# Optimization experiments

Hardware: AMD Instinct MI355X
Metric: run time of the kernel (lower is better)

The kernel has to match this reference:

```python
import jax, jax.numpy as jnp
import numpy as np

B, T, D, H, L, R, V = 4, 1024, 1024, 16, 12, 32, 50257
HD = D // H
SCALING = 2.0   # lora_alpha(64) / lora_rank(32) at the default 16-bit precision
EPS = 1e-5
KV_QMAX = float(2 ** 8 - 1)  # kv_cache_bits = 8 (middle of [4,8,16])


def _ln(x, g, b):
    m = jnp.mean(x, -1, keepdims=True)
    v = jnp.mean(jnp.square(x - m), -1, keepdims=True)
    return (x - m) * jax.lax.rsqrt(v + EPS) * g + b


def _round_ste(x):
    return x + jax.lax.stop_gradient(jnp.round(x) - x)


def _fake_quant(x, mn, mx):
    # asymmetric learnable fake-quant with straight-through rounding
    scale = (mx - mn) / KV_QMAX
    zp = _round_ste(-mn / scale)
    q = jnp.clip(_round_ste(x / scale) + zp, 0.0, KV_QMAX)
    return (q - zp) * scale


def _sp_linear(x, w, b, la, lb):
    # quantized-base linear (full precision at 16-bit) + LoRA adapter (eval: no dropout)
    return x @ w + b + SCALING * ((x @ la) @ lb)


def setup_inputs() -> dict:
    key = jax.random.key(0)
    ks = iter(jax.random.split(key, 64))
    rn = lambda shape, s=0.02: jax.random.normal(next(ks), shape, jnp.float32) * s
    return {
        "input_ids": jax.random.randint(next(ks), (B, T), 0, V),
        "wte": rn((V, D)), "wpe": rn((T, D)),
        "ln1_g": jnp.ones((L, D)), "ln1_b": jnp.zeros((L, D)),
        "attn_w": rn((L, D, 3 * D)), "attn_b": jnp.zeros((L, 3 * D)),
        "attn_la": rn((L, D, R)), "attn_lb": rn((L, R, 3 * D)),
        "proj_w": rn((L, D, D)), "proj_b": jnp.zeros((L, D)),
        "proj_la": rn((L, D, R)), "proj_lb": rn((L, R, D)),
        "ln2_g": jnp.ones((L, D)), "ln2_b": jnp.zeros((L, D)),
        "fc_w": rn((L, D, 4 * D)), "fc_b": jnp.zeros((L, 4 * D)),
        "fc_la": rn((L, D, R)), "fc_lb": rn((L, R, 4 * D)),
        "mproj_w": rn((L, 4 * D, D)), "mproj_b": jnp.zeros((L, D)),
        "mproj_la": rn((L, 4 * D, R)), "mproj_lb": rn((L, R, D)),
        "kv_min": jnp.full((L,), -4.0), "kv_max": jnp.full((L,), 4.0),
        "lnf_g": jnp.ones((D,)), "lnf_b": jnp.zeros((D,)),
    }


def reference(input_ids, wte, wpe, ln1_g, ln1_b, attn_w, attn_b, attn_la, attn_lb,
              proj_w, proj_b, proj_la, proj_lb, ln2_g, ln2_b, fc_w, fc_b, fc_la,
              fc_lb, mproj_w, mproj_b, mproj_la, mproj_lb, kv_min, kv_max,
              lnf_g, lnf_b):
    mask = jnp.tril(jnp.ones((T, T), bool))
    h = wte[input_ids] + wpe[None, :T]  # [B,T,D] (dropout is identity in eval)

    def block(h, p):
        (g1, b1, aw, ab, ala, alb, pw, pb, pla, plb, g2, b2,
         fw, fb, fla, flb, mw, mb, mla, mlb, mn, mx) = p
        x = _ln(h, g1, b1)
        qkv = _sp_linear(x, aw, ab, ala, alb)  # [B,T,3D]
        q, k, v = jnp.split(qkv, 3, axis=-1)
        heads = lambda t: t.reshape(B, T, H, HD).transpose(0, 2, 1, 3)  # bhtd
        q, k, v = heads(q), heads(k), heads(v)
        # KV-cache fake quantization (default precision flag unset on attn)
        k = _fake_quant(k, mn, mx)
        v = _fake_quant(v, mn, mx)
        att = jnp.einsum('bhqd,bhkd->bhqk', q, k) / np.float32(np.sqrt(HD))
        att = jax.nn.softmax(jnp.where(mask, att, -jnp.inf), axis=-1)
        o = jnp.einsum('bhqk,bhkd->bhqd', att, v).transpose(0, 2, 1, 3).reshape(B, T, D)
        h = h + _sp_linear(o, pw, pb, pla, plb)
        x = _ln(h, g2, b2)
        m = jax.nn.gelu(_sp_linear(x, fw, fb, fla, flb), approximate=False)
        h = h + _sp_linear(m, mw, mb, mla, mlb)
        return h, None

    params = (ln1_g, ln1_b, attn_w, attn_b, attn_la, attn_lb, proj_w, proj_b,
              proj_la, proj_lb, ln2_g, ln2_b, fc_w, fc_b, fc_la, fc_lb,
              mproj_w, mproj_b, mproj_la, mproj_lb, kv_min, kv_max)
    h, _ = jax.lax.scan(block, h, params)
    return _ln(h, lnf_g, lnf_b)
```

## Files before the change

kernel.cpp:

```cpp
#include <hip/hip_runtime.h>
#include <hip/hip_bf16.h>


typedef __bf16 bf16x8 __attribute__((ext_vector_type(8)));
typedef float f32x4 __attribute__((ext_vector_type(4)));

static __device__ __forceinline__ float bf2f(unsigned short u) {
    union { unsigned int i; float f; } c; c.i = ((unsigned int)u) << 16; return c.f;
}
static __device__ __forceinline__ unsigned short f2bf(float f) {
    unsigned int u = __float_as_uint(f);
    u += 0x7fffu + ((u >> 16) & 1u);
    return (unsigned short)(u >> 16);
}

#define GL2LDS(g, l) __builtin_amdgcn_global_load_lds( \
    (const __attribute__((address_space(1))) unsigned int*)(g), \
    (__attribute__((address_space(3))) unsigned int*)(l), 16, 0, 0)

__global__ __launch_bounds__(256) void k_embed(const int* __restrict__ ids,
        const float* __restrict__ wte, const float* __restrict__ wpe,
        float* __restrict__ h) {
    int row = blockIdx.x;
    int t = row & 1023;
    int id = ids[row];
    int d = threadIdx.x * 4;
    float4 a = *(const float4*)(wte + (size_t)id * 1024 + d);
    float4 b = *(const float4*)(wpe + (size_t)t * 1024 + d);
    float4 o = make_float4(a.x + b.x, a.y + b.y, a.z + b.z, a.w + b.w);
    *(float4*)(h + (size_t)row * 1024 + d) = o;
}

template <bool BF16OUT>
__global__ __launch_bounds__(256) void k_ln(const float* __restrict__ h,
        const float* __restrict__ g, const float* __restrict__ be,
        unsigned short* __restrict__ xo, float* __restrict__ fo) {
    int row = blockIdx.x, tid = threadIdx.x;
    float4 v = *(const float4*)(h + (size_t)row * 1024 + tid * 4);
    float s = v.x + v.y + v.z + v.w;
    for (int off = 32; off; off >>= 1) s += __shfl_down(s, off);
    __shared__ float red[8];
    int wid = tid >> 6, lane = tid & 63;
    if (!lane) red[wid] = s;
    __syncthreads();
    float mean = (red[0] + red[1] + red[2] + red[3]) * (1.f / 1024.f);
    float dx = v.x - mean, dy = v.y - mean, dz = v.z - mean, dw = v.w - mean;
    float q = dx * dx + dy * dy + dz * dz + dw * dw;
    for (int off = 32; off; off >>= 1) q += __shfl_down(q, off);
    if (!lane) red[4 + wid] = q;
    __syncthreads();
    float var = (red[4] + red[5] + red[6] + red[7]) * (1.f / 1024.f);
    float inv = 1.0f / sqrtf(var + 1e-5f);
    float4 gv = *(const float4*)(g + tid * 4);
    float4 bv = *(const float4*)(be + tid * 4);
    float y0 = dx * inv * gv.x + bv.x;
    float y1 = dy * inv * gv.y + bv.y;
    float y2 = dz * inv * gv.z + bv.z;
    float y3 = dw * inv * gv.w + bv.w;
    if (BF16OUT) {
        ushort4 o;
        o.x = f2bf(y0); o.y = f2bf(y1); o.z = f2bf(y2); o.w = f2bf(y3);
        *(ushort4*)(xo + (size_t)row * 1024 + tid * 4) = o;
    } else {
        *(float4*)(fo + (size_t)row * 1024 + tid * 4) = make_float4(y0, y1, y2, y3);
    }
}

__global__ __launch_bounds__(256) void k_lora_mfma(const unsigned short* __restrict__ A,
        const unsigned short* __restrict__ laT, unsigned short* __restrict__ tmp, int K) {
    int rowBase = blockIdx.x * 16;
    int tid = threadIdx.x, w = tid >> 6, lane = tid & 63;
    int lrow = lane & 15, lk8 = (lane >> 4) * 8;
    int kq = K >> 2;
    f32x4 acc0 = {0.f, 0.f, 0.f, 0.f}, acc1 = {0.f, 0.f, 0.f, 0.f};
    const unsigned short* arow = A + (size_t)(rowBase + lrow) * K + w * kq + lk8;
    const unsigned short* b0p = laT + (size_t)lrow * K + w * kq + lk8;
    const unsigned short* b1p = laT + (size_t)(16 + lrow) * K + w * kq + lk8;
#pragma unroll 2
    for (int kt = 0; kt < kq; kt += 32) {
        bf16x8 af = *(const bf16x8*)(arow + kt);
        bf16x8 b0 = *(const bf16x8*)(b0p + kt);
        bf16x8 b1 = *(const bf16x8*)(b1p + kt);
        acc0 = __builtin_amdgcn_mfma_f32_16x16x32_bf16(af, b0, acc0, 0, 0, 0);
        acc1 = __builtin_amdgcn_mfma_f32_16x16x32_bf16(af, b1, acc1, 0, 0, 0);
    }
    __shared__ f32x4 red[2][4][64];
    red[0][w][lane] = acc0;
    red[1][w][lane] = acc1;
    __syncthreads();
    if (w == 0) {
        acc0 = red[0][0][lane] + red[0][1][lane] + red[0][2][lane] + red[0][3][lane];
        acc1 = red[1][0][lane] + red[1][1][lane] + red[1][2][lane] + red[1][3][lane];
        int lq = lane >> 4;
#pragma unroll
        for (int rg = 0; rg < 4; ++rg) {
            int row = rowBase + lq * 4 + rg;
            tmp[(size_t)row * 64 + lrow] = f2bf(acc0[rg]);
            tmp[(size_t)row * 64 + 16 + lrow] = f2bf(acc1[rg]);
            tmp[(size_t)row * 64 + 32 + lrow] = 0;
            tmp[(size_t)row * 64 + 48 + lrow] = 0;
        }
    }
}

__global__ __launch_bounds__(256) void k_prep(
        const float* aw, const float* pw, const float* fw, const float* mw,
        const float* alb, const float* plb, const float* flb, const float* mlb,
        const float* ala, const float* pla, const float* fla, const float* mla,
        unsigned short* WTq, unsigned short* WTp, unsigned short* WTf, unsigned short* WTm,
        unsigned short* LTq, unsigned short* LTp, unsigned short* LTf, unsigned short* LTm,
        unsigned short* LAq, unsigned short* LAp, unsigned short* LAf, unsigned short* LAm) {
    int bid = blockIdx.x;
    const float* src; unsigned short* dst; int K, N, ntn, local, dstS; float scale = 1.f;
    if      (bid < 768)  { src = aw;  dst = WTq; K = 1024; N = 3072; ntn = 48; local = bid; dstS = K; }
    else if (bid < 1024) { src = pw;  dst = WTp; K = 1024; N = 1024; ntn = 16; local = bid - 768; dstS = K; }
    else if (bid < 2048) { src = fw;  dst = WTf; K = 1024; N = 4096; ntn = 64; local = bid - 1024; dstS = K; }
    else if (bid < 3072) { src = mw;  dst = WTm; K = 4096; N = 1024; ntn = 16; local = bid - 2048; dstS = K; }
    else if (bid < 3120) { src = alb; dst = LTq; K = 32;   N = 3072; ntn = 48; local = bid - 3072; scale = 2.f; dstS = 64; }
    else if (bid < 3136) { src = plb; dst = LTp; K = 32;   N = 1024; ntn = 16; local = bid - 3120; scale = 2.f; dstS = 64; }
    else if (bid < 3200) { src = flb; dst = LTf; K = 32;   N = 4096; ntn = 64; local = bid - 3136; scale = 2.f; dstS = 64; }
    else if (bid < 3216) { src = mlb; dst = LTm; K = 32;   N = 1024; ntn = 16; local = bid - 3200; scale = 2.f; dstS = 64; }
    else if (bid < 3232) { src = ala; dst = LAq; K = 1024; N = 32;   ntn = 1;  local = bid - 3216; dstS = K; }
    else if (bid < 3248) { src = pla; dst = LAp; K = 1024; N = 32;   ntn = 1;  local = bid - 3232; dstS = K; }
    else if (bid < 3264) { src = fla; dst = LAf; K = 1024; N = 32;   ntn = 1;  local = bid - 3248; dstS = K; }
    else                 { src = mla; dst = LAm; K = 4096; N = 32;   ntn = 1;  local = bid - 3264; dstS = K; }
    int kt = local / ntn, nt = local % ntn;
    int k0 = kt * 64, n0 = nt * 64;
    __shared__ unsigned short Tl[64][72];
    int tid = threadIdx.x;
    int cr = tid >> 6;
    int cc = tid & 63;
#pragma unroll
    for (int p = 0; p < 16; ++p) {
        int kl = p * 4 + cr;
        if (k0 + kl < K && n0 + cc < N) Tl[kl][cc] = f2bf(src[(size_t)(k0 + kl) * N + n0 + cc] * scale);
    }
    __syncthreads();
#pragma unroll
    for (int p = 0; p < 16; ++p) {
        int nl = p * 4 + cr;
        int kl = cc;
        if (n0 + nl < N) {
            if (k0 + kl < K) dst[(size_t)(n0 + nl) * dstS + k0 + kl] = Tl[kl][nl];
            else if (k0 + kl < dstS) dst[(size_t)(n0 + nl) * dstS + k0 + kl] = 0;
        }
    }
}

template <int EPI>
__global__ __launch_bounds__(128) void k_gemm64(
        const unsigned short* __restrict__ A, const unsigned short* __restrict__ WT,
        const float* __restrict__ bias, const unsigned short* __restrict__ tmpA,
        const unsigned short* __restrict__ lbT, const float* __restrict__ res,
        float* __restrict__ outF, int N, int K) {
    __shared__ unsigned short Al[128 * 32];
    __shared__ unsigned short Bl[64 * 32];
    int tid = threadIdx.x;
    int nBase = blockIdx.x * 64, rowBase = blockIdx.y * 128;
    int w = tid >> 6, lane = tid & 63;
    int lrow = lane & 15, lk8 = (lane >> 4) * 8;
    int srow = lane >> 2;
    int scol = (lane & 3) * 8;
    f32x4 acc[4][4];
#pragma unroll
    for (int i = 0; i < 4; ++i)
#pragma unroll
        for (int j = 0; j < 4; ++j) acc[i][j] = f32x4{0.f, 0.f, 0.f, 0.f};
    int nk = K >> 5;
    for (int kt = 0; kt <= nk; ++kt) {
        bool mn = kt < nk;
        const unsigned short* sa[4];
        const unsigned short* sb[2];
#pragma unroll
        for (int i = 0; i < 4; ++i) {
            int r = rowBase + w * 64 + i * 16 + srow;
            sa[i] = mn ? A + (size_t)r * K + kt * 32 + scol
                       : tmpA + (size_t)r * 64 + scol;
        }
#pragma unroll
        for (int i = 0; i < 2; ++i) {
            int r = nBase + w * 32 + i * 16 + srow;
            sb[i] = mn ? WT + (size_t)r * K + kt * 32 + scol
                       : lbT + (size_t)r * 64 + scol;
        }
        __syncthreads();
#pragma unroll
        for (int i = 0; i < 4; ++i) GL2LDS(sa[i], &Al[(w * 64 + i * 16) * 32]);
#pragma unroll
        for (int i = 0; i < 2; ++i) GL2LDS(sb[i], &Bl[(w * 32 + i * 16) * 32]);
        __syncthreads();
        bf16x8 af[4], bfr[4];
#pragma unroll
        for (int mt = 0; mt < 4; ++mt) af[mt] = *(const bf16x8*)&Al[(w * 64 + mt * 16 + lrow) * 32 + lk8];
#pragma unroll
        for (int nt = 0; nt < 4; ++nt) bfr[nt] = *(const bf16x8*)&Bl[(nt * 16 + lrow) * 32 + lk8];
#pragma unroll
        for (int mt = 0; mt < 4; ++mt)
#pragma unroll
            for (int nt = 0; nt < 4; ++nt)
                acc[mt][nt] = __builtin_amdgcn_mfma_f32_16x16x32_bf16(af[mt], bfr[nt], acc[mt][nt], 0, 0, 0);
    }
    int lq = lane >> 4;
#pragma unroll
    for (int nt = 0; nt < 4; ++nt) {
        int col = nBase + nt * 16 + lrow;
        float bv = bias[col];
#pragma unroll
        for (int mt = 0; mt < 4; ++mt) {
            int row0 = rowBase + w * 64 + mt * 16 + lq * 4;
#pragma unroll
            for (int rg = 0; rg < 4; ++rg) {
                int row = row0 + rg;
                float v = acc[mt][nt][rg] + bv;
                size_t idx = (size_t)row * N + col;
                if (EPI == 1) v += res[idx];
                outF[idx] = v;
            }
        }
    }
}

template <int EPI>
__global__ __launch_bounds__(512, 1) void k_gemm256(
        const unsigned short* __restrict__ A, const unsigned short* __restrict__ WT,
        const float* __restrict__ bias, const unsigned short* __restrict__ tmpA,
        const unsigned short* __restrict__ lbT,
        const float* __restrict__ kvmin, const float* __restrict__ kvmax, int layer,
        unsigned short* __restrict__ qh, unsigned short* __restrict__ kh,
        unsigned short* __restrict__ vh,
        float* __restrict__ outF, unsigned short* __restrict__ outH, int N, int K) {
    __shared__ unsigned short lds[9 * 8192];
    const int tid = threadIdx.x;
    const int wid = tid >> 6, lane = tid & 63;
    const int wr = wid >> 2, wc = wid & 3;
    const int nBase = blockIdx.x * 256, rowBase = blockIdx.y * 256;
    const int nk = (K >> 6) + 1;

    f32x4 acc[8][4];
#pragma unroll
    for (int i = 0; i < 8; ++i)
#pragma unroll
        for (int j = 0; j < 4; ++j) acc[i][j] = f32x4{0.f, 0.f, 0.f, 0.f};

    auto stage = [&](int s) {
        int kt = s >> 2, part = s & 3;
        bool dead = kt >= nk;
        unsigned short* dst = &lds[(dead ? 8 : (s & 7)) * 8192];
        bool isA = part >= 2;
        int half = part & 1;
        bool lora = (kt == nk - 1);
#pragma unroll
        for (int i = 0; i < 2; ++i) {
            int o = ((i * 8 + wid) << 10) + (lane << 4);
            int r = o >> 7;
            int col = ((o & 127) ^ (((o >> 9) & 3) << 5)) >> 1;
            const unsigned short* src;
            if (dead) {
                src = A + (lane << 3);
            } else if (isA) {
                int grow = rowBase + half * 128 + r;
                src = lora ? tmpA + (size_t)grow * 64 + col
                           : A + (size_t)grow * K + kt * 64 + col;
            } else {
                int gcol = nBase + half * 128 + r;
                src = lora ? lbT + (size_t)gcol * 64 + col
                           : WT + (size_t)gcol * K + kt * 64 + col;
            }
            GL2LDS(src, dst + ((i * 8 + wid) << 9));
        }
    };

    stage(0); stage(1); stage(2); stage(3);
    stage(4); stage(5); stage(6);
    asm volatile("s_waitcnt vmcnt(6)" ::: "memory");
    __builtin_amdgcn_s_barrier();

    for (int kt = 0; kt < nk; ++kt) {
        const unsigned short* aPart = &lds[(((kt & 1) << 2) + 2 + wr) * 8192];
        const unsigned short* bPart = &lds[(((kt & 1) << 2) + (wc >> 1)) * 8192];
        bf16x8 bfr[4][2];
#pragma unroll
        for (int p = 0; p < 4; ++p) {
            bf16x8 af[2][2];
#pragma unroll
            for (int mm = 0; mm < 2; ++mm)
#pragma unroll
                for (int kk = 0; kk < 2; ++kk) {
                    int row = (p * 2 + mm) * 16 + (lane & 15);
                    int cb = (kk * 64 + ((lane >> 4) << 4)) ^ (((row >> 2) & 3) << 5);
                    af[mm][kk] = *(const bf16x8*)&aPart[row * 64 + (cb >> 1)];
                }
            if (p == 0) {
#pragma unroll
                for (int n = 0; n < 4; ++n)
#pragma unroll
                    for (int kk = 0; kk < 2; ++kk) {
                        int row = ((wc & 1) << 6) + n * 16 + (lane & 15);
                        int cb = (kk * 64 + ((lane >> 4) << 4)) ^ (((row >> 2) & 3) << 5);
                        bfr[n][kk] = *(const bf16x8*)&bPart[row * 64 + (cb >> 1)];
                    }
            }
            stage(p == 0 ? 4 * (kt + 1) + 3 : 4 * (kt + 2) + (p - 1));
            __builtin_amdgcn_s_barrier();
            __builtin_amdgcn_s_setprio(1);
#pragma unroll
            for (int mm = 0; mm < 2; ++mm)
#pragma unroll
                for (int n = 0; n < 4; ++n)
#pragma unroll
                    for (int kk = 0; kk < 2; ++kk)
                        acc[p * 2 + mm][n] = __builtin_amdgcn_mfma_f32_16x16x32_bf16(
                            af[mm][kk], bfr[n][kk], acc[p * 2 + mm][n], 0, 0, 0);
            __builtin_amdgcn_s_setprio(0);
            if (p == 3) asm volatile("s_waitcnt vmcnt(6)" ::: "memory");
            __builtin_amdgcn_s_barrier();
        }
    }

    if (EPI == 3) {
        const int b = rowBase >> 10, t0 = rowBase & 1023;
        const int sec = nBase >> 10, nb = nBase & 1023;
        const int lrow = lane & 15, lq4 = (lane >> 4) << 2;
        float qs = 1.f, qzp = 0.f, qinv = 1.f;
        if (sec) {
            float mnv = kvmin[layer], mxv = kvmax[layer];
            qs = (mxv - mnv) * (1.f / 255.f);
            qzp = rintf(-mnv / qs);
            qinv = 1.f / qs;
        }
#pragma unroll
        for (int n = 0; n < 4; ++n) {
            int dd = wc * 64 + n * 16 + lrow;
            float bv = bias[nBase + dd];
#pragma unroll
            for (int m = 0; m < 8; ++m) {
#pragma unroll
                for (int rg = 0; rg < 4; ++rg) {
                    int tt = wr * 128 + m * 16 + lq4 + rg;
                    float v = acc[m][n][rg] + bv;
                    if (sec) {
                        float qv = rintf(v * qinv) + qzp;
                        qv = fminf(fmaxf(qv, 0.f), 255.f);
                        v = (qv - qzp) * qs;
                    }
                    int r = (sec == 2) ? dd : tt;
                    int c = (sec == 2) ? tt : dd;
                    lds[r * 256 + (c ^ ((r & 7) << 3))] = f2bf(v);
                }
            }
        }
        __syncthreads();
        if (sec < 2) {
            unsigned short* dstp = sec ? kh : qh;
            int tL = tid & 255;
            int hp = tid >> 8;
#pragma unroll
            for (int hi = 0; hi < 2; ++hi) {
                int dL = (hp * 2 + hi) * 64;
                int hh = (nb >> 6) + hp * 2 + hi;
                size_t base = (((size_t)(b * 16 + hh)) * 1024 + t0 + tL) * 64;
#pragma unroll
                for (int j = 0; j < 8; ++j) {
                    int c = (dL + j * 8) ^ ((tL & 7) << 3);
                    *(uint4*)(dstp + base + j * 8) = *(const uint4*)&lds[tL * 256 + c];
                }
            }
        } else {
            int dL = tid & 255;
            int th = (tid >> 8) * 128;
            int hh = (nb >> 6) + (dL >> 6);
            size_t base = (((size_t)(b * 16 + hh)) * 64 + (dL & 63)) * 1024 + t0 + th;
#pragma unroll
            for (int j = 0; j < 16; ++j) {
                int c = (th + j * 8) ^ ((dL & 7) << 3);
                *(uint4*)(vh + base + j * 8) = *(const uint4*)&lds[dL * 256 + c];
            }
        }
    } else {
#pragma unroll
        for (int n = 0; n < 4; ++n) {
            int col = nBase + wc * 64 + n * 16 + (lane & 15);
            float bv = bias[col];
#pragma unroll
            for (int m = 0; m < 8; ++m) {
                int row0 = rowBase + wr * 128 + m * 16 + ((lane >> 4) << 2);
#pragma unroll
                for (int rg = 0; rg < 4; ++rg) {
                    int row = row0 + rg;
                    float v = acc[m][n][rg] + bv;
                    size_t idx = (size_t)row * N + col;
                    if (EPI == 2) {
                        v = 0.5f * v * (1.f + erff(v * 0.70710678118654752f));
                        outH[idx] = f2bf(v);
                    } else {
                        outF[idx] = v;
                    }
                }
            }
        }
    }
}

__global__ __launch_bounds__(256) void k_attn(const unsigned short* __restrict__ qh,
        const unsigned short* __restrict__ kh, const unsigned short* __restrict__ vh,
        unsigned short* __restrict__ o) {
    int fid = blockIdx.y * 16 + blockIdx.x;
    int wgid = (fid & 7) * 128 + (fid >> 3);
    int bh = wgid >> 4, qb = wgid & 15;
    int b = bh >> 4, hh = bh & 15;
    int tid = threadIdx.x, w = tid >> 6, lane = tid & 63;
    int cq = lane & 15;
    int g = lane >> 4;
    int lk8 = g * 8;
    __shared__ unsigned short Kl[64][72];
    __shared__ unsigned short Vt[64][72];
    __shared__ unsigned short Pl[4][16][72];
    const float SCL = 0.18033688011112042f;
    int qrow = qb * 64 + w * 16 + cq;
    bf16x8 aq[2];
    aq[0] = *(const bf16x8*)(qh + ((size_t)bh * 1024 + qrow) * 64 + lk8);
    aq[1] = *(const bf16x8*)(qh + ((size_t)bh * 1024 + qrow) * 64 + 32 + lk8);
    f32x4 od[4];
#pragma unroll
    for (int i = 0; i < 4; ++i) od[i] = f32x4{0.f, 0.f, 0.f, 0.f};
    float mrun = -3e38f, lrun = 0.f;
    int rl = tid >> 2, seg = (tid & 3) * 16;
    for (int kb = 0; kb <= qb; ++kb) {
        __syncthreads();
        {
            size_t kbase = ((size_t)bh * 1024 + kb * 64 + rl) * 64 + seg;
            *(uint4*)&Kl[rl][seg] = *(const uint4*)(kh + kbase);
            *(uint4*)&Kl[rl][seg + 8] = *(const uint4*)(kh + kbase + 8);
            size_t vbase = ((size_t)bh * 64 + rl) * 1024 + kb * 64 + seg;
            *(uint4*)&Vt[rl][seg] = *(const uint4*)(vh + vbase);
            *(uint4*)&Vt[rl][seg + 8] = *(const uint4*)(vh + vbase + 8);
        }
        __syncthreads();
        f32x4 st[4];
#pragma unroll
        for (int ktile = 0; ktile < 4; ++ktile) {
            f32x4 sacc = f32x4{0.f, 0.f, 0.f, 0.f};
#pragma unroll
            for (int dh = 0; dh < 2; ++dh) {
                bf16x8 bk = *(const bf16x8*)&Kl[ktile * 16 + cq][dh * 32 + lk8];
                sacc = __builtin_amdgcn_mfma_f32_16x16x32_bf16(bk, aq[dh], sacc, 0, 0, 0);
            }
            st[ktile] = sacc * SCL;
        }
        if (kb == qb) {
#pragma unroll
            for (int ktile = 0; ktile < 4; ++ktile) {
#pragma unroll
                for (int rg = 0; rg < 4; ++rg) {
                    int kidx = kb * 64 + ktile * 16 + g * 4 + rg;
                    if (kidx > qrow) st[ktile][rg] = -3e38f;
                }
            }
        }
        float pmax = st[0][0];
#pragma unroll
        for (int ktile = 0; ktile < 4; ++ktile)
#pragma unroll
            for (int rg = 0; rg < 4; ++rg) pmax = fmaxf(pmax, st[ktile][rg]);
        pmax = fmaxf(pmax, __shfl_xor(pmax, 16));
        pmax = fmaxf(pmax, __shfl_xor(pmax, 32));
        float mnew = fmaxf(mrun, pmax);
        float sum = 0.f;
#pragma unroll
        for (int ktile = 0; ktile < 4; ++ktile)
#pragma unroll
            for (int rg = 0; rg < 4; ++rg) {
                st[ktile][rg] = exp2f(st[ktile][rg] - mnew);
                sum += st[ktile][rg];
            }
        sum += __shfl_xor(sum, 16);
        sum += __shfl_xor(sum, 32);
        float corr = exp2f(mrun - mnew);
        lrun = lrun * corr + sum;
        mrun = mnew;
#pragma unroll
        for (int rg = 0; rg < 4; ++rg) {
            float cv = __shfl(corr, (lane & 48) | (g * 4 + rg));
#pragma unroll
            for (int dt = 0; dt < 4; ++dt) od[dt][rg] *= cv;
        }
#pragma unroll
        for (int ktile = 0; ktile < 4; ++ktile) {
            ushort4 pw;
            pw.x = f2bf(st[ktile][0]); pw.y = f2bf(st[ktile][1]);
            pw.z = f2bf(st[ktile][2]); pw.w = f2bf(st[ktile][3]);
            *(ushort4*)&Pl[w][cq][ktile * 16 + g * 4] = pw;
        }
        bf16x8 pa[2];
        pa[0] = *(const bf16x8*)&Pl[w][cq][lk8];
        pa[1] = *(const bf16x8*)&Pl[w][cq][32 + lk8];
#pragma unroll
        for (int dt = 0; dt < 4; ++dt) {
#pragma unroll
            for (int kh2 = 0; kh2 < 2; ++kh2) {
                bf16x8 bv = *(const bf16x8*)&Vt[dt * 16 + cq][kh2 * 32 + lk8];
                od[dt] = __builtin_amdgcn_mfma_f32_16x16x32_bf16(pa[kh2], bv, od[dt], 0, 0, 0);
            }
        }
    }
#pragma unroll
    for (int rg = 0; rg < 4; ++rg) {
        float lv = __shfl(lrun, (lane & 48) | (g * 4 + rg));
        float inv = 1.0f / lv;
        int row = qb * 64 + w * 16 + g * 4 + rg;
#pragma unroll
        for (int dt = 0; dt < 4; ++dt) {
            float val = od[dt][rg] * inv;
            o[((size_t)(b * 1024 + row)) * 1024 + hh * 64 + dt * 16 + cq] = f2bf(val);
        }
    }
}

extern "C" void kernel_launch(void* const* d_in, const int* in_sizes, int n_in,
                              void* d_out, int out_size, void* d_ws, size_t ws_size,
                              hipStream_t stream) {
    const int*   ids      = (const int*)d_in[0];
    const float* wte      = (const float*)d_in[1];
    const float* wpe      = (const float*)d_in[2];
    const float* ln1_g    = (const float*)d_in[3];
    const float* ln1_b    = (const float*)d_in[4];
    const float* attn_w   = (const float*)d_in[5];
    const float* attn_b   = (const float*)d_in[6];
    const float* attn_la  = (const float*)d_in[7];
    const float* attn_lb  = (const float*)d_in[8];
    const float* proj_w   = (const float*)d_in[9];
    const float* proj_b   = (const float*)d_in[10];
    const float* proj_la  = (const float*)d_in[11];
    const float* proj_lb  = (const float*)d_in[12];
    const float* ln2_g    = (const float*)d_in[13];
    const float* ln2_b    = (const float*)d_in[14];
    const float* fc_w     = (const float*)d_in[15];
    const float* fc_b     = (const float*)d_in[16];
    const float* fc_la    = (const float*)d_in[17];
    const float* fc_lb    = (const float*)d_in[18];
    const float* mproj_w  = (const float*)d_in[19];
    const float* mproj_b  = (const float*)d_in[20];
    const float* mproj_la = (const float*)d_in[21];
    const float* mproj_lb = (const float*)d_in[22];
    const float* kv_min   = (const float*)d_in[23];
    const float* kv_max   = (const float*)d_in[24];
    const float* lnf_g    = (const float*)d_in[25];
    const float* lnf_b    = (const float*)d_in[26];

    char* ws = (char*)d_ws;
    size_t off = 0;
    auto alloc = [&](size_t bytes) -> char* {
        char* p = ws + off;
        off = (off + bytes + 255) & ~(size_t)255;
        return p;
    };
    float*          h   = (float*)alloc(4096ull * 1024 * 4);
    unsigned short* xb  = (unsigned short*)alloc(4096ull * 1024 * 2);
    unsigned short* tmp = (unsigned short*)alloc(4096ull * 64 * 2);
    unsigned short* qhb = (unsigned short*)alloc(64ull * 1024 * 64 * 2);
    unsigned short* khb = (unsigned short*)alloc(64ull * 1024 * 64 * 2);
    unsigned short* vhb = (unsigned short*)alloc(64ull * 64 * 1024 * 2);
    unsigned short* ob  = (unsigned short*)alloc(4096ull * 1024 * 2);
    unsigned short* mb  = (unsigned short*)alloc(4096ull * 4096 * 2);
    unsigned short* WTq = (unsigned short*)alloc(3072ull * 1024 * 2);
    unsigned short* WTp = (unsigned short*)alloc(1024ull * 1024 * 2);
    unsigned short* WTf = (unsigned short*)alloc(4096ull * 1024 * 2);
    unsigned short* WTm = (unsigned short*)alloc(1024ull * 4096 * 2);
    unsigned short* LTq = (unsigned short*)alloc(3072ull * 64 * 2);
    unsigned short* LTp = (unsigned short*)alloc(1024ull * 64 * 2);
    unsigned short* LTf = (unsigned short*)alloc(4096ull * 64 * 2);
    unsigned short* LTm = (unsigned short*)alloc(1024ull * 64 * 2);
    unsigned short* LAq = (unsigned short*)alloc(32ull * 1024 * 2);
    unsigned short* LAp = (unsigned short*)alloc(32ull * 1024 * 2);
    unsigned short* LAf = (unsigned short*)alloc(32ull * 1024 * 2);
    unsigned short* LAm = (unsigned short*)alloc(32ull * 4096 * 2);

    k_embed<<<4096, 256, 0, stream>>>(ids, wte, wpe, h);
    for (int l = 0; l < 12; ++l) {
        k_prep<<<3328, 256, 0, stream>>>(
            attn_w + (size_t)l * 1024 * 3072, proj_w + (size_t)l * 1024 * 1024,
            fc_w + (size_t)l * 1024 * 4096, mproj_w + (size_t)l * 4096 * 1024,
            attn_lb + (size_t)l * 32 * 3072, proj_lb + (size_t)l * 32 * 1024,
            fc_lb + (size_t)l * 32 * 4096, mproj_lb + (size_t)l * 32 * 1024,
            attn_la + (size_t)l * 1024 * 32, proj_la + (size_t)l * 1024 * 32,
            fc_la + (size_t)l * 1024 * 32, mproj_la + (size_t)l * 4096 * 32,
            WTq, WTp, WTf, WTm, LTq, LTp, LTf, LTm, LAq, LAp, LAf, LAm);
        k_ln<true><<<4096, 256, 0, stream>>>(h, ln1_g + l * 1024, ln1_b + l * 1024, xb, nullptr);
        k_lora_mfma<<<256, 256, 0, stream>>>(xb, LAq, tmp, 1024);
        k_gemm256<3><<<dim3(12, 16), 512, 0, stream>>>(xb, WTq, attn_b + l * 3072, tmp, LTq,
                                                       kv_min, kv_max, l, qhb, khb, vhb,
                                                       nullptr, nullptr, 3072, 1024);
        k_attn<<<dim3(16, 64), 256, 0, stream>>>(qhb, khb, vhb, ob);
        k_lora_mfma<<<256, 256, 0, stream>>>(ob, LAp, tmp, 1024);
        k_gemm64<1><<<dim3(16, 32), 128, 0, stream>>>(ob, WTp, proj_b + l * 1024, tmp, LTp,
                                                      h, h, 1024, 1024);
        k_ln<true><<<4096, 256, 0, stream>>>(h, ln2_g + l * 1024, ln2_b + l * 1024, xb, nullptr);
        k_lora_mfma<<<256, 256, 0, stream>>>(xb, LAf, tmp, 1024);
        k_gemm256<2><<<dim3(16, 16), 512, 0, stream>>>(xb, WTf, fc_b + l * 4096, tmp, LTf,
                                                       nullptr, nullptr, 0, nullptr, nullptr, nullptr,
                                                       nullptr, mb, 4096, 1024);
        k_lora_mfma<<<256, 256, 0, stream>>>(mb, LAm, tmp, 4096);
        k_gemm64<1><<<dim3(16, 32), 128, 0, stream>>>(mb, WTm, mproj_b + l * 1024, tmp, LTm,
                                                      h, h, 1024, 4096);
    }
    k_ln<false><<<4096, 256, 0, stream>>>(h, lnf_g, lnf_b, nullptr, (float*)d_out);
}
```

Baseline: 4.265 ms.

## Batch weight prep for all layers into one launch and widen gemm64 to 256 threads

Moves the per-layer weight transpose and bf16 conversion out of the layer loop into a single 2D-grid launch that prepares all 12 layers up front, using per-layer workspace buffers. This removes 11 serialized prep launches and lets the prep run as one large, fully parallel kernel. Separately, the 128x64 gemm kernel now runs with 4 waves of 32 rows each instead of 2 waves of 64 rows, halving accumulators per wave to raise occupancy and latency hiding. The cost is about 12x more workspace memory for the converted weights.

```diff
diff --git a/kernel.cpp b/kernel.cpp
--- a/kernel.cpp
+++ b/kernel.cpp
@@ -104,26 +104,27 @@
 }
 
 __global__ __launch_bounds__(256) void k_prep(
-        const float* aw, const float* pw, const float* fw, const float* mw,
-        const float* alb, const float* plb, const float* flb, const float* mlb,
-        const float* ala, const float* pla, const float* fla, const float* mla,
-        unsigned short* WTq, unsigned short* WTp, unsigned short* WTf, unsigned short* WTm,
-        unsigned short* LTq, unsigned short* LTp, unsigned short* LTf, unsigned short* LTm,
-        unsigned short* LAq, unsigned short* LAp, unsigned short* LAf, unsigned short* LAm) {
+        const float* awB, const float* pwB, const float* fwB, const float* mwB,
+        const float* albB, const float* plbB, const float* flbB, const float* mlbB,
+        const float* alaB, const float* plaB, const float* flaB, const float* mlaB,
+        unsigned short* WTqB, unsigned short* WTpB, unsigned short* WTfB, unsigned short* WTmB,
+        unsigned short* LTqB, unsigned short* LTpB, unsigned short* LTfB, unsigned short* LTmB,
+        unsigned short* LAqB, unsigned short* LApB, unsigned short* LAfB, unsigned short* LAmB) {
     int bid = blockIdx.x;
+    size_t l = blockIdx.y;
     const float* src; unsigned short* dst; int K, N, ntn, local, dstS; float scale = 1.f;
-    if      (bid < 768)  { src = aw;  dst = WTq; K = 1024; N = 3072; ntn = 48; local = bid; dstS = K; }
-    else if (bid < 1024) { src = pw;  dst = WTp; K = 1024; N = 1024; ntn = 16; local = bid - 768; dstS = K; }
-    else if (bid < 2048) { src = fw;  dst = WTf; K = 1024; N = 4096; ntn = 64; local = bid - 1024; dstS = K; }
-    else if (bid < 3072) { src = mw;  dst = WTm; K = 4096; N = 1024; ntn = 16; local = bid - 2048; dstS = K; }
-    else if (bid < 3120) { src = alb; dst = LTq; K = 32;   N = 3072; ntn = 48; local = bid - 3072; scale = 2.f; dstS = 64; }
-    else if (bid < 3136) { src = plb; dst = LTp; K = 32;   N = 1024; ntn = 16; local = bid - 3120; scale = 2.f; dstS = 64; }
-    else if (bid < 3200) { src = flb; dst = LTf; K = 32;   N = 4096; ntn = 64; local = bid - 3136; scale = 2.f; dstS = 64; }
-    else if (bid < 3216) { src = mlb; dst = LTm; K = 32;   N = 1024; ntn = 16; local = bid - 3200; scale = 2.f; dstS = 64; }
-    else if (bid < 3232) { src = ala; dst = LAq; K = 1024; N = 32;   ntn = 1;  local = bid - 3216; dstS = K; }
-    else if (bid < 3248) { src = pla; dst = LAp; K = 1024; N = 32;   ntn = 1;  local = bid - 3232; dstS = K; }
-    else if (bid < 3264) { src = fla; dst = LAf; K = 1024; N = 32;   ntn = 1;  local = bid - 3248; dstS = K; }
-    else                 { src = mla; dst = LAm; K = 4096; N = 32;   ntn = 1;  local = bid - 3264; dstS = K; }
+    if      (bid < 768)  { src = awB + l*3145728;  dst = WTqB + l*3145728; K = 1024; N = 3072; ntn = 48; local = bid; dstS = K; }
+    else if (bid < 1024) { src = pwB + l*1048576;  dst = WTpB + l*1048576; K = 1024; N = 1024; ntn = 16; local = bid - 768; dstS = K; }
+    else if (bid < 2048) { src = fwB + l*4194304;  dst = WTfB + l*4194304; K = 1024; N = 4096; ntn = 64; local = bid - 1024; dstS = K; }
+    else if (bid < 3072) { src = mwB + l*4194304;  dst = WTmB + l*4194304; K = 4096; N = 1024; ntn = 16; local = bid - 2048; dstS = K; }
+    else if (bid < 3120) { src = albB + l*98304;   dst = LTqB + l*196608;  K = 32;   N = 3072; ntn = 48; local = bid - 3072; scale = 2.f; dstS = 64; }
+    else if (bid < 3136) { src = plbB + l*32768;   dst = LTpB + l*65536;   K = 32;   N = 1024; ntn = 16; local = bid - 3120; scale = 2.f; dstS = 64; }
+    else if (bid < 3200) { src = flbB + l*131072;  dst = LTfB + l*262144;  K = 32;   N = 4096; ntn = 64; local = bid - 3136; scale = 2.f; dstS = 64; }
+    else if (bid < 3216) { src = mlbB + l*32768;   dst = LTmB + l*65536;   K = 32;   N = 1024; ntn = 16; local = bid - 3200; scale = 2.f; dstS = 64; }
+    else if (bid < 3232) { src = alaB + l*32768;   dst = LAqB + l*32768;   K = 1024; N = 32;   ntn = 1;  local = bid - 3216; dstS = K; }
+    else if (bid < 3248) { src = plaB + l*32768;   dst = LApB + l*32768;   K = 1024; N = 32;   ntn = 1;  local = bid - 3232; dstS = K; }
+    else if (bid < 3264) { src = flaB + l*32768;   dst = LAfB + l*32768;   K = 1024; N = 32;   ntn = 1;  local = bid - 3248; dstS = K; }
+    else                 { src = mlaB + l*131072;  dst = LAmB + l*131072;  K = 4096; N = 32;   ntn = 1;  local = bid - 3264; dstS = K; }
     int kt = local / ntn, nt = local % ntn;
     int k0 = kt * 64, n0 = nt * 64;
     __shared__ unsigned short Tl[64][72];
@@ -148,7 +149,7 @@
 }
 
 template <int EPI>
-__global__ __launch_bounds__(128) void k_gemm64(
+__global__ __launch_bounds__(256) void k_gemm64(
         const unsigned short* __restrict__ A, const unsigned short* __restrict__ WT,
         const float* __restrict__ bias, const unsigned short* __restrict__ tmpA,
         const unsigned short* __restrict__ lbT, const float* __restrict__ res,
@@ -161,41 +162,39 @@
     int lrow = lane & 15, lk8 = (lane >> 4) * 8;
     int srow = lane >> 2;
     int scol = (lane & 3) * 8;
-    f32x4 acc[4][4];
-#pragma unroll
-    for (int i = 0; i < 4; ++i)
+    f32x4 acc[2][4];
+#pragma unroll
+    for (int i = 0; i < 2; ++i)
 #pragma unroll
         for (int j = 0; j < 4; ++j) acc[i][j] = f32x4{0.f, 0.f, 0.f, 0.f};
     int nk = K >> 5;
     for (int kt = 0; kt <= nk; ++kt) {
         bool mn = kt < nk;
-        const unsigned short* sa[4];
-        const unsigned short* sb[2];
-#pragma unroll
-        for (int i = 0; i < 4; ++i) {
-            int r = rowBase + w * 64 + i * 16 + srow;
+        const unsigned short* sa[2];
+        const unsigned short* sb;
+#pragma unroll
+        for (int i = 0; i < 2; ++i) {
+            int r = rowBase + w * 32 + i * 16 + srow;
             sa[i] = mn ? A + (size_t)r * K + kt * 32 + scol
                        : tmpA + (size_t)r * 64 + scol;
         }
-#pragma unroll
-        for (int i = 0; i < 2; ++i) {
-            int r = nBase + w * 32 + i * 16 + srow;
-            sb[i] = mn ? WT + (size_t)r * K + kt * 32 + scol
-                       : lbT + (size_t)r * 64 + scol;
+        {
+            int r = nBase + w * 16 + srow;
+            sb = mn ? WT + (size_t)r * K + kt * 32 + scol
+                    : lbT + (size_t)r * 64 + scol;
         }
         __syncthreads();
 #pragma unroll
-        for (int i = 0; i < 4; ++i) GL2LDS(sa[i], &Al[(w * 64 + i * 16) * 32]);
-#pragma unroll
-        for (int i = 0; i < 2; ++i) GL2LDS(sb[i], &Bl[(w * 32 + i * 16) * 32]);
+        for (int i = 0; i < 2; ++i) GL2LDS(sa[i], &Al[(w * 32 + i * 16) * 32]);
+        GL2LDS(sb, &Bl[(w * 16) * 32]);
         __syncthreads();
-        bf16x8 af[4], bfr[4];
-#pragma unroll
-        for (int mt = 0; mt < 4; ++mt) af[mt] = *(const bf16x8*)&Al[(w * 64 + mt * 16 + lrow) * 32 + lk8];
+        bf16x8 af[2], bfr[4];
+#pragma unroll
+        for (int mt = 0; mt < 2; ++mt) af[mt] = *(const bf16x8*)&Al[(w * 32 + mt * 16 + lrow) * 32 + lk8];
 #pragma unroll
         for (int nt = 0; nt < 4; ++nt) bfr[nt] = *(const bf16x8*)&Bl[(nt * 16 + lrow) * 32 + lk8];
 #pragma unroll
-        for (int mt = 0; mt < 4; ++mt)
+        for (int mt = 0; mt < 2; ++mt)
 #pragma unroll
             for (int nt = 0; nt < 4; ++nt)
                 acc[mt][nt] = __builtin_amdgcn_mfma_f32_16x16x32_bf16(af[mt], bfr[nt], acc[mt][nt], 0, 0, 0);
@@ -206,8 +205,8 @@
         int col = nBase + nt * 16 + lrow;
         float bv = bias[col];
 #pragma unroll
-        for (int mt = 0; mt < 4; ++mt) {
-            int row0 = rowBase + w * 64 + mt * 16 + lq * 4;
+        for (int mt = 0; mt < 2; ++mt) {
+            int row0 = rowBase + w * 32 + mt * 16 + lq * 4;
 #pragma unroll
             for (int rg = 0; rg < 4; ++rg) {
                 int row = row0 + rg;
@@ -562,45 +561,46 @@
     unsigned short* vhb = (unsigned short*)alloc(64ull * 64 * 1024 * 2);
     unsigned short* ob  = (unsigned short*)alloc(4096ull * 1024 * 2);
     unsigned short* mb  = (unsigned short*)alloc(4096ull * 4096 * 2);
-    unsigned short* WTq = (unsigned short*)alloc(3072ull * 1024 * 2);
-    unsigned short* WTp = (unsigned short*)alloc(1024ull * 1024 * 2);
-    unsigned short* WTf = (unsigned short*)alloc(4096ull * 1024 * 2);
-    unsigned short* WTm = (unsigned short*)alloc(1024ull * 4096 * 2);
-    unsigned short* LTq = (unsigned short*)alloc(3072ull * 64 * 2);
-    unsigned short* LTp = (unsigned short*)alloc(1024ull * 64 * 2);
-    unsigned short* LTf = (unsigned short*)alloc(4096ull * 64 * 2);
-    unsigned short* LTm = (unsigned short*)alloc(1024ull * 64 * 2);
-    unsigned short* LAq = (unsigned short*)alloc(32ull * 1024 * 2);
-    unsigned short* LAp = (unsigned short*)alloc(32ull * 1024 * 2);
-    unsigned short* LAf = (unsigned short*)alloc(32ull * 1024 * 2);
-    unsigned short* LAm = (unsigned short*)alloc(32ull * 4096 * 2);
+    unsigned short* WTq = (unsigned short*)alloc(12ull * 3072 * 1024 * 2);
+    unsigned short* WTp = (unsigned short*)alloc(12ull * 1024 * 1024 * 2);
+    unsigned short* WTf = (unsigned short*)alloc(12ull * 4096 * 1024 * 2);
+    unsigned short* WTm = (unsigned short*)alloc(12ull * 1024 * 4096 * 2);
+    unsigned short* LTq = (unsigned short*)alloc(12ull * 3072 * 64 * 2);
+    unsigned short* LTp = (unsigned short*)alloc(12ull * 1024 * 64 * 2);
+    unsigned short* LTf = (unsigned short*)alloc(12ull * 4096 * 64 * 2);
+    unsigned short* LTm = (unsigned short*)alloc(12ull * 1024 * 64 * 2);
+    unsigned short* LAq = (unsigned short*)alloc(12ull * 32 * 1024 * 2);
+    unsigned short* LAp = (unsigned short*)alloc(12ull * 32 * 1024 * 2);
+    unsigned short* LAf = (unsigned short*)alloc(12ull * 32 * 1024 * 2);
+    unsigned short* LAm = (unsigned short*)alloc(12ull * 32 * 4096 * 2);
 
     k_embed<<<4096, 256, 0, stream>>>(ids, wte, wpe, h);
+    k_prep<<<dim3(3328, 12), 256, 0, stream>>>(
+        attn_w, proj_w, fc_w, mproj_w,
+        attn_lb, proj_lb, fc_lb, mproj_lb,
+        attn_la, proj_la, fc_la, mproj_la,
+        WTq, WTp, WTf, WTm, LTq, LTp, LTf, LTm, LAq, LAp, LAf, LAm);
     for (int l = 0; l < 12; ++l) {
-        k_prep<<<3328, 256, 0, stream>>>(
-            attn_w + (size_t)l * 1024 * 3072, proj_w + (size_t)l * 1024 * 1024,
-            fc_w + (size_t)l * 1024 * 4096, mproj_w + (size_t)l * 4096 * 1024,
-            attn_lb + (size_t)l * 32 * 3072, proj_lb + (size_t)l * 32 * 1024,
-            fc_lb + (size_t)l * 32 * 4096, mproj_lb + (size_t)l * 32 * 1024,
-            attn_la + (size_t)l * 1024 * 32, proj_la + (size_t)l * 1024 * 32,
-            fc_la + (size_t)l * 1024 * 32, mproj_la + (size_t)l * 4096 * 32,
-            WTq, WTp, WTf, WTm, LTq, LTp, LTf, LTm, LAq, LAp, LAf, LAm);
         k_ln<true><<<4096, 256, 0, stream>>>(h, ln1_g + l * 1024, ln1_b + l * 1024, xb, nullptr);
-        k_lora_mfma<<<256, 256, 0, stream>>>(xb, LAq, tmp, 1024);
-        k_gemm256<3><<<dim3(12, 16), 512, 0, stream>>>(xb, WTq, attn_b + l * 3072, tmp, LTq,
+        k_lora_mfma<<<256, 256, 0, stream>>>(xb, LAq + (size_t)l * 32768, tmp, 1024);
+        k_gemm256<3><<<dim3(12, 16), 512, 0, stream>>>(xb, WTq + (size_t)l * 3145728,
+                                                       attn_b + l * 3072, tmp, LTq + (size_t)l * 196608,
                                                        kv_min, kv_max, l, qhb, khb, vhb,
                                                        nullptr, nullptr, 3072, 1024);
         k_attn<<<dim3(16, 64), 256, 0, stream>>>(qhb, khb, vhb, ob);
-        k_lora_mfma<<<256, 256, 0, stream>>>(ob, LAp, tmp, 1024);
-        k_gemm64<1><<<dim3(16, 32), 128, 0, stream>>>(ob, WTp, proj_b + l * 1024, tmp, LTp,
+        k_lora_mfma<<<256, 256, 0, stream>>>(ob, LAp + (size_t)l * 32768, tmp, 1024);
+        k_gemm64<1><<<dim3(16, 32), 256, 0, stream>>>(ob, WTp + (size_t)l * 1048576,
+                                                      proj_b + l * 1024, tmp, LTp + (size_t)l * 65536,
                                                       h, h, 1024, 1024);
         k_ln<true><<<4096, 256, 0, stream>>>(h, ln2_g + l * 1024, ln2_b + l * 1024, xb, nullptr);
-        k_lora_mfma<<<256, 256, 0, stream>>>(xb, LAf, tmp, 1024);
-        k_gemm256<2><<<dim3(16, 16), 512, 0, stream>>>(xb, WTf, fc_b + l * 4096, tmp, LTf,
+        k_lora_mfma<<<256, 256, 0, stream>>>(xb, LAf + (size_t)l * 32768, tmp, 1024);
+        k_gemm256<2><<<dim3(16, 16), 512, 0, stream>>>(xb, WTf + (size_t)l * 4194304,
+                                                       fc_b + l * 4096, tmp, LTf + (size_t)l * 262144,
                                                        nullptr, nullptr, 0, nullptr, nullptr, nullptr,
                                                        nullptr, mb, 4096, 1024);
-        k_lora_mfma<<<256, 256, 0, stream>>>(mb, LAm, tmp, 4096);
-        k_gemm64<1><<<dim3(16, 32), 128, 0, stream>>>(mb, WTm, mproj_b + l * 1024, tmp, LTm,
+        k_lora_mfma<<<256, 256, 0, stream>>>(mb, LAm + (size_t)l * 131072, tmp, 4096);
+        k_gemm64<1><<<dim3(16, 32), 256, 0, stream>>>(mb, WTm + (size_t)l * 4194304,
+                                                      mproj_b + l * 1024, tmp, LTm + (size_t)l * 65536,
                                                       h, h, 1024, 4096);
     }
     k_ln<false><<<4096, 256, 0, stream>>>(h, lnf_g, lnf_b, nullptr, (float*)d_out);
```

After: 4.204 ms. Within noise of the previous version (-1.4%).
